# Kernel optimization log

Hardware: AMD Instinct MI355X
Metric: run time of the kernel (lower is better)

Reference implementation:

```python
import jax, jax.numpy as jnp
import numpy as np

B, M, E, IN, Q, OUT, H = 256, 2048, 128, 512, 512, 512, 64

def _lin(x, w, b):
    return x @ w.T + b

def setup_inputs() -> dict:
    key = jax.random.key(0)
    ks = jax.random.split(key, 20)
    d = {
        'read_weights': jax.random.uniform(ks[0], (B, M)),
        'write_weights': jax.random.uniform(ks[1], (B, M)),
        'usage': jax.random.uniform(ks[2], (B, M)),
        'free_gates': jax.random.uniform(ks[3], (B, M)),
        'x': jax.random.normal(ks[4], (B, 1, IN)),
        'query': jax.random.normal(ks[5], (B, 1, Q)),
        'memory': jax.random.normal(ks[6], (B, M, E)),
        'I_w': jax.random.normal(ks[7], (E, IN)) * 0.02, 'I_b': jnp.zeros((E,)),
        'W1_w': jax.random.normal(ks[8], (H, E)) * 0.02, 'W1_b': jnp.zeros((H,)),
        'W2_w': jax.random.normal(ks[9], (H, E)) * 0.02, 'W2_b': jnp.zeros((H,)),
        'R1_w': jax.random.normal(ks[10], (H, Q)) * 0.02, 'R1_b': jnp.zeros((H,)),
        'R2_w': jax.random.normal(ks[11], (H, E)) * 0.02, 'R2_b': jnp.zeros((H,)),
        'O_w': jax.random.normal(ks[12], (OUT, E)) * 0.02, 'O_b': jnp.zeros((OUT,)),
    }
    return d

def _allocation(read_weights, write_weights, usage, free_gates):
    u = 1e-5 + (1.0 - 1e-5) * usage
    psi = 1.0 - free_gates * read_weights
    u = u + write_weights - u * write_weights
    u = u * psi                                   # new usage [B, M]
    phi = jnp.argsort(u, axis=1)                  # ascending order indices
    sorted_u = jnp.take_along_axis(u, phi, axis=1)
    # NOTE: original uses inclusive cumprod (matches torch code exactly)
    sorted_alloc = (1.0 - sorted_u) * jnp.cumprod(sorted_u, axis=1)
    phi_rev = jnp.argsort(phi, axis=1)            # inverse permutation
    alloc = jnp.take_along_axis(sorted_alloc, phi_rev, axis=1)
    return u, alloc

def reference(read_weights, write_weights, usage, free_gates, x, query, memory,
              I_w, I_b, W1_w, W1_b, W2_w, W2_b, R1_w, R1_b, R2_w, R2_b, O_w, O_b):
    # ---- write ----
    emb = _lin(x, I_w, I_b)                       # [B,1,E]
    Wi = _lin(emb, W1_w, W1_b)                    # [B,1,H]
    Wm = _lin(memory, W2_w, W2_b)                 # [B,M,H]
    scores = jnp.einsum('bqh,bmh->bqm', Wi, Wm)   # [B,1,M]
    w_content = jax.nn.softmax(scores, axis=2)
    new_usage, alloc = _allocation(read_weights, write_weights, usage, free_gates)
    w = (w_content + alloc[:, None, :]) * 0.5     # [B,1,M]
    new_memory = memory + w.transpose(0, 2, 1) * emb  # [B,M,1]*[B,1,E]
    new_write_weights = w[:, 0, :]
    # ---- read ----
    Rq = _lin(query, R1_w, R1_b)                  # [B,1,H]
    Rm = _lin(new_memory, R2_w, R2_b)             # [B,M,H]
    rscores = jnp.einsum('bqh,bmh->bqm', Rq, Rm)
    wr = jax.nn.softmax(rscores, axis=2)          # [B,1,M]
    pooled = jnp.einsum('bm,bme->be', wr[:, 0, :], new_memory)
    output = _lin(pooled, O_w, O_b)               # [B,OUT]
    return ((wr[:, 0, :], new_write_weights, new_usage), output, new_memory)
```

## Files before the change

### kernel.cpp

```cpp
#include <hip/hip_runtime.h>
#include <hip/hip_bf16.h>

constexpr int B   = 256;
constexpr int M   = 2048;
constexpr int E   = 128;
constexpr int IN  = 512;
constexpr int Qd  = 512;
constexpr int OUTd= 512;
constexpr int H   = 64;

constexpr size_t OFF_WR = 0;
constexpr size_t OFF_W  = (size_t)B*M;
constexpr size_t OFF_U  = (size_t)2*B*M;
constexpr size_t OFF_Y  = (size_t)3*B*M;
constexpr size_t OFF_NM = OFF_Y + (size_t)B*OUTd;

__device__ __forceinline__ float bf2f(unsigned short u) {
    union { unsigned int i; float f; } v; v.i = ((unsigned int)u) << 16; return v.f;
}
__device__ __forceinline__ unsigned short f2bf(float f) {
    unsigned int x = __float_as_uint(f);
    unsigned int r = (x + 0x7fffu + ((x >> 16) & 1u)) >> 16;
    return (unsigned short)r;
}
__device__ __forceinline__ void unpack8(uint4 d, float* o) {
    o[0]=bf2f(d.x & 0xffff); o[1]=bf2f(d.x >> 16);
    o[2]=bf2f(d.y & 0xffff); o[3]=bf2f(d.y >> 16);
    o[4]=bf2f(d.z & 0xffff); o[5]=bf2f(d.z >> 16);
    o[6]=bf2f(d.w & 0xffff); o[7]=bf2f(d.w >> 16);
}
__device__ __forceinline__ uint4 pack8(const float* f) {
    uint4 d;
    d.x = (unsigned)f2bf(f[0]) | ((unsigned)f2bf(f[1]) << 16);
    d.y = (unsigned)f2bf(f[2]) | ((unsigned)f2bf(f[3]) << 16);
    d.z = (unsigned)f2bf(f[4]) | ((unsigned)f2bf(f[5]) << 16);
    d.w = (unsigned)f2bf(f[6]) | ((unsigned)f2bf(f[7]) << 16);
    return d;
}

__device__ __forceinline__ float ldf(const void* p, size_t i, int bf) {
    return bf ? bf2f(((const unsigned short*)p)[i]) : ((const float*)p)[i];
}
__device__ __forceinline__ void ld8(const void* p, size_t i, int bf, float* o) {
    if (bf) {
        uint4 d = *(const uint4*)((const unsigned short*)p + i);
        unpack8(d, o);
    } else {
        const float4* q = (const float4*)((const float*)p + i);
        float4 a = q[0], c = q[1];
        o[0]=a.x; o[1]=a.y; o[2]=a.z; o[3]=a.w;
        o[4]=c.x; o[5]=c.y; o[6]=c.z; o[7]=c.w;
    }
}
__device__ __forceinline__ void st1(void* p, size_t i, int bf, float v) {
    if (bf) ((unsigned short*)p)[i] = f2bf(v);
    else    ((float*)p)[i] = v;
}
__device__ __forceinline__ void st8(void* p, size_t i, int bf, const float* v) {
    if (bf) {
        *(uint4*)((unsigned short*)p + i) = pack8(v);
    } else {
        float4 a, c;
        a.x=v[0]; a.y=v[1]; a.z=v[2]; a.w=v[3];
        c.x=v[4]; c.y=v[5]; c.z=v[6]; c.w=v[7];
        float4* q = (float4*)((float*)p + i);
        q[0]=a; q[1]=c;
    }
}

__device__ __forceinline__ int detect_bf(const void* usage) {
    const int lane = threadIdx.x & 63;
    uint4 d = ((const uint4*)usage)[lane];
    float o[8]; unpack8(d, o);
    bool ok = true;
    #pragma unroll
    for (int j = 0; j < 8; ++j) ok = ok && (o[j] >= 0.0f && o[j] <= 1.0f);
    unsigned long long m = __ballot(ok);
    return (__popcll(m) >= 32) ? 1 : 0;
}

__device__ __forceinline__ float bmax4(float v, float* r4, int t) {
    #pragma unroll
    for (int m = 1; m < 64; m <<= 1) v = fmaxf(v, __shfl_xor(v, m, 64));
    __syncthreads();
    if ((t & 63) == 0) r4[t >> 6] = v;
    __syncthreads();
    return fmaxf(fmaxf(r4[0], r4[1]), fmaxf(r4[2], r4[3]));
}
__device__ __forceinline__ float bsum4(float v, float* r4, int t) {
    #pragma unroll
    for (int m = 1; m < 64; m <<= 1) v += __shfl_xor(v, m, 64);
    __syncthreads();
    if ((t & 63) == 0) r4[t >> 6] = v;
    __syncthreads();
    return (r4[0] + r4[1]) + (r4[2] + r4[3]);
}

__global__ __launch_bounds__(256) void kA_pre_alloc(
    const void* __restrict__ x,   const void* __restrict__ qy,
    const void* __restrict__ I_w, const void* __restrict__ I_b,
    const void* __restrict__ W1w, const void* __restrict__ W1b,
    const void* __restrict__ W2w, const void* __restrict__ W2b,
    const void* __restrict__ R1w, const void* __restrict__ R1b,
    const void* __restrict__ R2w, const void* __restrict__ R2b,
    const void* __restrict__ rw,  const void* __restrict__ ww,
    const void* __restrict__ us,  const void* __restrict__ fg,
    float* __restrict__ emb_ws, float* __restrict__ v_ws, float* __restrict__ u2_ws,
    float* __restrict__ c1_ws,  float* __restrict__ c2_ws, float* __restrict__ d2_ws,
    float* __restrict__ alloc_ws, void* __restrict__ dout)
{
    __shared__ unsigned long long sh64[M];
    __shared__ float scan[256];
    const int bf = detect_bf(us);
    const int t = threadIdx.x;

    if (blockIdx.x < B) {
        const int b = blockIdx.x;
        float* fsm  = (float*)sh64;
        float* xs   = fsm;
        float* qs   = fsm + 512;
        float* embs = fsm + 1024;
        float* wis  = fsm + 1152;
        float* rqs  = fsm + 1216;
        float* red  = scan;
        float uu = 0.f;

        for (int i = t; i < IN; i += 256) xs[i] = ldf(x,  (size_t)b*IN + i, bf);
        for (int i = t; i < Qd; i += 256) qs[i] = ldf(qy, (size_t)b*Qd + i, bf);
        __syncthreads();

        if (t < 128) {
            float acc = 0.f;
            for (int c = 0; c < IN/8; ++c) {
                float m8[8]; ld8(I_w, (size_t)t*IN + c*8, bf, m8);
                #pragma unroll
                for (int j = 0; j < 8; ++j) acc += m8[j] * xs[c*8 + j];
            }
            acc += ldf(I_b, t, bf);
            embs[t] = acc;
            emb_ws[(size_t)b*E + t] = acc;
        } else {
            int t2 = t - 128;
            if (t2 < H) {
                float rv = 0.f;
                for (int c = 0; c < Qd/8; ++c) {
                    float m8[8]; ld8(R1w, (size_t)t2*Qd + c*8, bf, m8);
                    #pragma unroll
                    for (int j = 0; j < 8; ++j) rv += m8[j] * qs[c*8 + j];
                }
                rv += ldf(R1b, t2, bf);
                rqs[t2] = rv;
            }
        }
        __syncthreads();

        if (t < H) {
            float wv = 0.f;
            for (int c = 0; c < E/8; ++c) {
                float m8[8]; ld8(W1w, (size_t)t*E + c*8, bf, m8);
                #pragma unroll
                for (int j = 0; j < 8; ++j) wv += m8[j] * embs[c*8 + j];
            }
            wv += ldf(W1b, t, bf);
            wis[t] = wv;
        } else if (t >= 128) {
            int t2 = t - 128;
            for (int h = 0; h < H; ++h) uu += ldf(R2w, (size_t)h*E + t2, bf) * rqs[h];
            u2_ws[(size_t)b*E + t2] = uu;
            red[t] = (t2 < H) ? rqs[t2] * ldf(R2b, t2, bf) : 0.f;
        }
        __syncthreads();

        if (t < 128) {
            float vv = 0.f;
            for (int h = 0; h < H; ++h) vv += ldf(W2w, (size_t)h*E + t, bf) * wis[h];
            v_ws[(size_t)b*E + t] = vv;
            red[t] = (t < H) ? wis[t] * ldf(W2b, t, bf) : 0.f;
        }
        __syncthreads();

        for (int off = 64; off > 0; off >>= 1) {
            if (t < off) red[t] += red[t + off];
            if (t >= 128 && t < 128 + off) red[t] += red[t + off];
            __syncthreads();
        }
        if (t == 0)   c1_ws[b] = red[0];
        if (t == 128) c2_ws[b] = red[128];
        __syncthreads();

        red[t] = (t >= 128) ? uu * embs[t - 128] : 0.f;
        __syncthreads();
        for (int off = 64; off > 0; off >>= 1) {
            if (t >= 128 && t < 128 + off) red[t] += red[t + off];
            __syncthreads();
        }
        if (t == 128) d2_ws[b] = red[128];

    } else {
        const int b = blockIdx.x - B;
        const size_t base = (size_t)b*M + (size_t)t*8;
        float r8[8], w8[8], u8[8], f8[8], nu[8];
        ld8(rw, base, bf, r8); ld8(ww, base, bf, w8);
        ld8(us, base, bf, u8); ld8(fg, base, bf, f8);

        unsigned long long key[8];
        #pragma unroll
        for (int q = 0; q < 8; ++q) {
            float u = 1e-5f + (1.0f - 1e-5f) * u8[q];
            float psi = 1.0f - f8[q] * r8[q];
            u = u + w8[q] - u * w8[q];
            u = u * psi;
            nu[q] = u;
            unsigned fb = __float_as_uint(u);
            fb = (fb & 0x80000000u) ? ~fb : (fb | 0x80000000u);
            key[q] = ((unsigned long long)fb << 32) | (unsigned)(t*8 + q);
        }
        st8(dout, OFF_U + base, bf, nu);

        for (int k = 2; k <= M; k <<= 1) {
            for (int j = k >> 1; j > 0; j >>= 1) {
                if (j >= 512) {
                    __syncthreads();
                    #pragma unroll
                    for (int q = 0; q < 8; ++q) sh64[t*8 + q] = key[q];
                    __syncthreads();
                    const bool up      = (((t << 3) & k) == 0);
                    const bool lower   = (((t << 3) & j) == 0);
                    const bool keepmin = (lower == up);
                    #pragma unroll
                    for (int q = 0; q < 8; ++q) {
                        unsigned long long o = sh64[(t*8 + q) ^ j];
                        bool take = keepmin ? (o < key[q]) : (o > key[q]);
                        if (take) key[q] = o;
                    }
                } else if (j >= 8) {
                    const int d = j >> 3;
                    const bool up      = (((t << 3) & k) == 0);
                    const bool keepmin = (((t & d) == 0) == up);
                    #pragma unroll
                    for (int q = 0; q < 8; ++q) {
                        unsigned long long o = __shfl_xor(key[q], d, 64);
                        bool take = keepmin ? (o < key[q]) : (o > key[q]);
                        if (take) key[q] = o;
                    }
                } else {
                    #pragma unroll
                    for (int q = 0; q < 8; ++q) {
                        if (!(q & j)) {
                            int p = q | j;
                            bool up = ((((t << 3) + q) & k) == 0);
                            unsigned long long a = key[q], c = key[p];
                            bool sw = up ? (a > c) : (a < c);
                            if (sw) { key[q] = c; key[p] = a; }
                        }
                    }
                }
            }
        }

        float su[8], lp[8]; int sidx[8];
        #pragma unroll
        for (int q = 0; q < 8; ++q) {
            unsigned fb = (unsigned)(key[q] >> 32);
            fb = (fb & 0x80000000u) ? (fb ^ 0x80000000u) : ~fb;
            su[q]   = __uint_as_float(fb);
            sidx[q] = (int)(key[q] & 0xffffffffu);
        }
        float run = 1.f;
        #pragma unroll
        for (int q = 0; q < 8; ++q) { run *= su[q]; lp[q] = run; }
        scan[t] = run;
        __syncthreads();
        for (int off = 1; off < 256; off <<= 1) {
            float val = scan[t];
            float oth = (t >= off) ? scan[t - off] : 1.0f;
            __syncthreads();
            scan[t] = val * oth;
            __syncthreads();
        }
        float pref = (t > 0) ? scan[t - 1] : 1.0f;
        #pragma unroll
        for (int q = 0; q < 8; ++q)
            alloc_ws[(size_t)b*M + sidx[q]] = (1.0f - su[q]) * (pref * lp[q]);
    }
}

__global__ __launch_bounds__(256) void kS_scores(
    const void* __restrict__ mem, const void* __restrict__ us,
    const float* __restrict__ v_ws, const float* __restrict__ u2_ws,
    const float* __restrict__ c1_ws,
    float* __restrict__ s1, float* __restrict__ s2)
{
    const int bf = detect_bf(us);
    const int blk = blockIdx.x;
    const int b = blk >> 4, chunk = blk & 15;
    const int t = threadIdx.x, l = t & 15, g = t >> 4;
    float v8[8], u8[8];
    {
        const float* vb = v_ws  + (size_t)b*E + l*8;
        const float* ub = u2_ws + (size_t)b*E + l*8;
        #pragma unroll
        for (int j = 0; j < 8; ++j) { v8[j] = vb[j]; u8[j] = ub[j]; }
    }
    const float cc1 = c1_ws[b];
    const size_t mbase = (size_t)b*M*E;
    const int row0 = chunk*128 + g;
    for (int it = 0; it < 8; ++it) {
        int row = row0 + it*16;
        float m8[8]; ld8(mem, mbase + (size_t)row*E + l*8, bf, m8);
        float p1 = 0.f, p2 = 0.f;
        #pragma unroll
        for (int j = 0; j < 8; ++j) { p1 += m8[j]*v8[j]; p2 += m8[j]*u8[j]; }
        #pragma unroll
        for (int mask = 8; mask > 0; mask >>= 1) {
            p1 += __shfl_xor(p1, mask, 16);
            p2 += __shfl_xor(p2, mask, 16);
        }
        if (l == 0) {
            s1[(size_t)b*M + row] = p1 + cc1;
            s2[(size_t)b*M + row] = p2;
        }
    }
}

__global__ __launch_bounds__(256) void kU_update(
    const void* __restrict__ mem, const void* __restrict__ us,
    const float* __restrict__ emb_ws, const float* __restrict__ alloc_ws,
    const float* __restrict__ s1, const float* __restrict__ s2,
    const float* __restrict__ c2_ws, const float* __restrict__ d2_ws,
    float* __restrict__ pooled_p, void* __restrict__ dout)
{
    __shared__ float wsh[M];
    __shared__ float wrsh[M];
    __shared__ float pw[4][E];
    __shared__ float r4[4];
    const int bf = detect_bf(us);
    const int rblk = (B*16 - 1) - (int)blockIdx.x;
    const int b = rblk >> 4, chunk = rblk & 15;
    const int t = threadIdx.x, l = t & 15, g = t >> 4;

    const float* s1b = s1 + (size_t)b*M;
    const float* s2b = s2 + (size_t)b*M;
    float sv[8];
    float lmax = -3.4e38f;
    #pragma unroll
    for (int s = 0; s < 8; ++s) { sv[s] = s1b[s*256 + t]; lmax = fmaxf(lmax, sv[s]); }
    float gmax = bmax4(lmax, r4, t);
    float lsum = 0.f;
    #pragma unroll
    for (int s = 0; s < 8; ++s) { float e = expf(sv[s] - gmax); sv[s] = e; lsum += e; }
    float inv = 1.0f / bsum4(lsum, r4, t);

    const float dd = d2_ws[b], cc = c2_ws[b];
    float rs[8];
    #pragma unroll
    for (int s = 0; s < 8; ++s) {
        int m = s*256 + t;
        float wv = 0.5f * (sv[s] * inv + alloc_ws[(size_t)b*M + m]);
        wsh[m] = wv;
        rs[s] = s2b[m] + wv * dd + cc;
        if (chunk == 0) st1(dout, OFF_W + (size_t)b*M + m, bf, wv);
    }

    lmax = -3.4e38f;
    #pragma unroll
    for (int s = 0; s < 8; ++s) lmax = fmaxf(lmax, rs[s]);
    gmax = bmax4(lmax, r4, t);
    lsum = 0.f;
    #pragma unroll
    for (int s = 0; s < 8; ++s) { float e = expf(rs[s] - gmax); rs[s] = e; lsum += e; }
    float inv2 = 1.0f / bsum4(lsum, r4, t);
    #pragma unroll
    for (int s = 0; s < 8; ++s) {
        int m = s*256 + t;
        float wrv = rs[s] * inv2;
        wrsh[m] = wrv;
        if (chunk == 0) st1(dout, OFF_WR + (size_t)b*M + m, bf, wrv);
    }
    __syncthreads();

    float e8[8];
    {
        const float* eb = emb_ws + (size_t)b*E + l*8;
        #pragma unroll
        for (int j = 0; j < 8; ++j) e8[j] = eb[j];
    }
    float acc[8] = {0,0,0,0,0,0,0,0};
    const size_t mbase = (size_t)b*M*E;
    const int row0 = chunk*128 + g;
    for (int it = 0; it < 8; ++it) {
        int row = row0 + it*16;
        size_t off = mbase + (size_t)row*E + l*8;
        float m8[8]; ld8(mem, off, bf, m8);
        const float wv  = wsh[row];
        const float wrv = wrsh[row];
        float n8[8];
        #pragma unroll
        for (int j = 0; j < 8; ++j) {
            n8[j] = m8[j] + wv * e8[j];
            acc[j] += wrv * n8[j];
        }
        st8(dout, OFF_NM + off, bf, n8);
    }
    #pragma unroll
    for (int j = 0; j < 8; ++j) {
        acc[j] += __shfl_xor(acc[j], 16, 64);
        acc[j] += __shfl_xor(acc[j], 32, 64);
    }
    const int wid = t >> 6;
    if ((t & 63) < 16) {
        const int l0 = t & 15;
        #pragma unroll
        for (int j = 0; j < 8; ++j) pw[wid][l0*8 + j] = acc[j];
    }
    __syncthreads();
    if (t < E)
        pooled_p[((size_t)b*16 + chunk)*E + t] = pw[0][t] + pw[1][t] + pw[2][t] + pw[3][t];
}

__global__ __launch_bounds__(512) void kO_out(
    const float* __restrict__ pooled_p,
    const void* __restrict__ O_w, const void* __restrict__ O_b,
    const void* __restrict__ us, void* __restrict__ dout)
{
    __shared__ float ps[E];
    const int bf = detect_bf(us);
    const int b = blockIdx.x, t = threadIdx.x;
    if (t < E) {
        float s = 0.f;
        #pragma unroll
        for (int c = 0; c < 16; ++c) s += pooled_p[((size_t)b*16 + c)*E + t];
        ps[t] = s;
    }
    __syncthreads();
    float a = 0.f;
    for (int c = 0; c < E/8; ++c) {
        float m8[8]; ld8(O_w, (size_t)t*E + c*8, bf, m8);
        #pragma unroll
        for (int j = 0; j < 8; ++j) a += m8[j] * ps[c*8 + j];
    }
    a += ldf(O_b, t, bf);
    st1(dout, OFF_Y + (size_t)b*OUTd + t, bf, a);
}

extern "C" void kernel_launch(void* const* d_in, const int* in_sizes, int n_in,
                              void* d_out, int out_size, void* d_ws, size_t ws_size,
                              hipStream_t stream)
{
    const void* rw  = d_in[0];
    const void* ww  = d_in[1];
    const void* us  = d_in[2];
    const void* fg  = d_in[3];
    const void* x   = d_in[4];
    const void* qy  = d_in[5];
    const void* mem = d_in[6];
    const void* I_w = d_in[7];
    const void* I_b = d_in[8];
    const void* W1w = d_in[9];
    const void* W1b = d_in[10];
    const void* W2w = d_in[11];
    const void* W2b = d_in[12];
    const void* R1w = d_in[13];
    const void* R1b = d_in[14];
    const void* R2w = d_in[15];
    const void* R2b = d_in[16];
    const void* O_w = d_in[17];
    const void* O_b = d_in[18];

    float* fbase    = (float*)d_ws;
    float* emb_ws   = fbase;
    float* v_ws     = emb_ws + (size_t)B*E;
    float* u2_ws    = v_ws   + (size_t)B*E;
    float* c1_ws    = u2_ws  + (size_t)B*E;
    float* c2_ws    = c1_ws  + B;
    float* d2_ws    = c2_ws  + B;
    float* alloc_ws = d2_ws  + B;
    float* s1_ws    = alloc_ws + (size_t)B*M;
    float* s2_ws    = s1_ws    + (size_t)B*M;
    float* pooled_p = s2_ws    + (size_t)B*M;

    kA_pre_alloc<<<2*B, 256, 0, stream>>>(x, qy, I_w, I_b, W1w, W1b, W2w, W2b,
                                          R1w, R1b, R2w, R2b, rw, ww, us, fg,
                                          emb_ws, v_ws, u2_ws, c1_ws, c2_ws, d2_ws,
                                          alloc_ws, d_out);
    kS_scores<<<B*16, 256, 0, stream>>>(mem, us, v_ws, u2_ws, c1_ws, s1_ws, s2_ws);
    kU_update<<<B*16, 256, 0, stream>>>(mem, us, emb_ws, alloc_ws, s1_ws, s2_ws,
                                        c2_ws, d2_ws, pooled_p, d_out);
    kO_out   <<<B,    512, 0, stream>>>(pooled_p, O_w, O_b, us, d_out);
}
```

Before: 670.9 us.

## Restructure pipeline: overlap allocation sort with score pass, precompute softmax stats

Splits the projection prologue into its own kernel and merges the per-batch allocation sort with the memory score pass in one launch, so sorting blocks run alongside streaming blocks. Softmax max and normalizer for both the write and read weights are computed once per batch in a new small stats kernel. The update kernel then no longer re-reduces all 2048 scores in each of its 16 chunk blocks; each block only evaluates its own 128 rows. This adds one extra launch and a small read of the score arrays in exchange for removing redundant per-chunk reductions and large shared-memory buffers.

```diff
diff --git a/kernel.cpp b/kernel.cpp
--- a/kernel.cpp
+++ b/kernel.cpp
@@ -96,18 +96,102 @@
     return (r4[0] + r4[1]) + (r4[2] + r4[3]);
 }
 
-__global__ __launch_bounds__(256) void kA_pre_alloc(
+__global__ __launch_bounds__(256) void k1_pre(
     const void* __restrict__ x,   const void* __restrict__ qy,
     const void* __restrict__ I_w, const void* __restrict__ I_b,
     const void* __restrict__ W1w, const void* __restrict__ W1b,
     const void* __restrict__ W2w, const void* __restrict__ W2b,
     const void* __restrict__ R1w, const void* __restrict__ R1b,
     const void* __restrict__ R2w, const void* __restrict__ R2b,
-    const void* __restrict__ rw,  const void* __restrict__ ww,
-    const void* __restrict__ us,  const void* __restrict__ fg,
+    const void* __restrict__ us,
     float* __restrict__ emb_ws, float* __restrict__ v_ws, float* __restrict__ u2_ws,
-    float* __restrict__ c1_ws,  float* __restrict__ c2_ws, float* __restrict__ d2_ws,
-    float* __restrict__ alloc_ws, void* __restrict__ dout)
+    float* __restrict__ c1_ws,  float* __restrict__ c2_ws, float* __restrict__ d2_ws)
+{
+    const int bf = detect_bf(us);
+    __shared__ float xs[IN], qs[Qd], embs[E], wis[H], rqs[H], red[256];
+    const int b = blockIdx.x, t = threadIdx.x;
+    float uu = 0.f;
+
+    for (int i = t; i < IN; i += 256) xs[i] = ldf(x,  (size_t)b*IN + i, bf);
+    for (int i = t; i < Qd; i += 256) qs[i] = ldf(qy, (size_t)b*Qd + i, bf);
+    __syncthreads();
+
+    if (t < 128) {
+        float acc = 0.f;
+        for (int c = 0; c < IN/8; ++c) {
+            float m8[8]; ld8(I_w, (size_t)t*IN + c*8, bf, m8);
+            #pragma unroll
+            for (int j = 0; j < 8; ++j) acc += m8[j] * xs[c*8 + j];
+        }
+        acc += ldf(I_b, t, bf);
+        embs[t] = acc;
+        emb_ws[(size_t)b*E + t] = acc;
+    } else {
+        int t2 = t - 128;
+        if (t2 < H) {
+            float rv = 0.f;
+            for (int c = 0; c < Qd/8; ++c) {
+                float m8[8]; ld8(R1w, (size_t)t2*Qd + c*8, bf, m8);
+                #pragma unroll
+                for (int j = 0; j < 8; ++j) rv += m8[j] * qs[c*8 + j];
+            }
+            rv += ldf(R1b, t2, bf);
+            rqs[t2] = rv;
+        }
+    }
+    __syncthreads();
+
+    if (t < H) {
+        float wv = 0.f;
+        for (int c = 0; c < E/8; ++c) {
+            float m8[8]; ld8(W1w, (size_t)t*E + c*8, bf, m8);
+            #pragma unroll
+            for (int j = 0; j < 8; ++j) wv += m8[j] * embs[c*8 + j];
+        }
+        wv += ldf(W1b, t, bf);
+        wis[t] = wv;
+    } else if (t >= 128) {
+        int t2 = t - 128;
+        for (int h = 0; h < H; ++h) uu += ldf(R2w, (size_t)h*E + t2, bf) * rqs[h];
+        u2_ws[(size_t)b*E + t2] = uu;
+        red[t] = (t2 < H) ? rqs[t2] * ldf(R2b, t2, bf) : 0.f;
+    }
+    __syncthreads();
+
+    if (t < 128) {
+        float vv = 0.f;
+        for (int h = 0; h < H; ++h) vv += ldf(W2w, (size_t)h*E + t, bf) * wis[h];
+        v_ws[(size_t)b*E + t] = vv;
+        red[t] = (t < H) ? wis[t] * ldf(W2b, t, bf) : 0.f;
+    }
+    __syncthreads();
+
+    for (int off = 64; off > 0; off >>= 1) {
+        if (t < off) red[t] += red[t + off];
+        if (t >= 128 && t < 128 + off) red[t] += red[t + off];
+        __syncthreads();
+    }
+    if (t == 0)   c1_ws[b] = red[0];
+    if (t == 128) c2_ws[b] = red[128];
+    __syncthreads();
+
+    red[t] = (t >= 128) ? uu * embs[t - 128] : 0.f;
+    __syncthreads();
+    for (int off = 64; off > 0; off >>= 1) {
+        if (t >= 128 && t < 128 + off) red[t] += red[t + off];
+        __syncthreads();
+    }
+    if (t == 128) d2_ws[b] = red[128];
+}
+
+__global__ __launch_bounds__(256) void kB_alloc_scores(
+    const void* __restrict__ rw, const void* __restrict__ ww,
+    const void* __restrict__ us, const void* __restrict__ fg,
+    const void* __restrict__ mem,
+    const float* __restrict__ v_ws, const float* __restrict__ u2_ws,
+    const float* __restrict__ c1_ws,
+    float* __restrict__ alloc_ws, float* __restrict__ s1, float* __restrict__ s2,
+    void* __restrict__ dout)
 {
     __shared__ unsigned long long sh64[M];
     __shared__ float scan[256];
@@ -116,88 +200,6 @@
 
     if (blockIdx.x < B) {
         const int b = blockIdx.x;
-        float* fsm  = (float*)sh64;
-        float* xs   = fsm;
-        float* qs   = fsm + 512;
-        float* embs = fsm + 1024;
-        float* wis  = fsm + 1152;
-        float* rqs  = fsm + 1216;
-        float* red  = scan;
-        float uu = 0.f;
-
-        for (int i = t; i < IN; i += 256) xs[i] = ldf(x,  (size_t)b*IN + i, bf);
-        for (int i = t; i < Qd; i += 256) qs[i] = ldf(qy, (size_t)b*Qd + i, bf);
-        __syncthreads();
-
-        if (t < 128) {
-            float acc = 0.f;
-            for (int c = 0; c < IN/8; ++c) {
-                float m8[8]; ld8(I_w, (size_t)t*IN + c*8, bf, m8);
-                #pragma unroll
-                for (int j = 0; j < 8; ++j) acc += m8[j] * xs[c*8 + j];
-            }
-            acc += ldf(I_b, t, bf);
-            embs[t] = acc;
-            emb_ws[(size_t)b*E + t] = acc;
-        } else {
-            int t2 = t - 128;
-            if (t2 < H) {
-                float rv = 0.f;
-                for (int c = 0; c < Qd/8; ++c) {
-                    float m8[8]; ld8(R1w, (size_t)t2*Qd + c*8, bf, m8);
-                    #pragma unroll
-                    for (int j = 0; j < 8; ++j) rv += m8[j] * qs[c*8 + j];
-                }
-                rv += ldf(R1b, t2, bf);
-                rqs[t2] = rv;
-            }
-        }
-        __syncthreads();
-
-        if (t < H) {
-            float wv = 0.f;
-            for (int c = 0; c < E/8; ++c) {
-                float m8[8]; ld8(W1w, (size_t)t*E + c*8, bf, m8);
-                #pragma unroll
-                for (int j = 0; j < 8; ++j) wv += m8[j] * embs[c*8 + j];
-            }
-            wv += ldf(W1b, t, bf);
-            wis[t] = wv;
-        } else if (t >= 128) {
-            int t2 = t - 128;
-            for (int h = 0; h < H; ++h) uu += ldf(R2w, (size_t)h*E + t2, bf) * rqs[h];
-            u2_ws[(size_t)b*E + t2] = uu;
-            red[t] = (t2 < H) ? rqs[t2] * ldf(R2b, t2, bf) : 0.f;
-        }
-        __syncthreads();
-
-        if (t < 128) {
-            float vv = 0.f;
-            for (int h = 0; h < H; ++h) vv += ldf(W2w, (size_t)h*E + t, bf) * wis[h];
-            v_ws[(size_t)b*E + t] = vv;
-            red[t] = (t < H) ? wis[t] * ldf(W2b, t, bf) : 0.f;
-        }
-        __syncthreads();
-
-        for (int off = 64; off > 0; off >>= 1) {
-            if (t < off) red[t] += red[t + off];
-            if (t >= 128 && t < 128 + off) red[t] += red[t + off];
-            __syncthreads();
-        }
-        if (t == 0)   c1_ws[b] = red[0];
-        if (t == 128) c2_ws[b] = red[128];
-        __syncthreads();
-
-        red[t] = (t >= 128) ? uu * embs[t - 128] : 0.f;
-        __syncthreads();
-        for (int off = 64; off > 0; off >>= 1) {
-            if (t >= 128 && t < 128 + off) red[t] += red[t + off];
-            __syncthreads();
-        }
-        if (t == 128) d2_ws[b] = red[128];
-
-    } else {
-        const int b = blockIdx.x - B;
         const size_t base = (size_t)b*M + (size_t)t*8;
         float r8[8], w8[8], u8[8], f8[8], nu[8];
         ld8(rw, base, bf, r8); ld8(ww, base, bf, w8);
@@ -282,100 +284,115 @@
         #pragma unroll
         for (int q = 0; q < 8; ++q)
             alloc_ws[(size_t)b*M + sidx[q]] = (1.0f - su[q]) * (pref * lp[q]);
-    }
-}
-
-__global__ __launch_bounds__(256) void kS_scores(
-    const void* __restrict__ mem, const void* __restrict__ us,
-    const float* __restrict__ v_ws, const float* __restrict__ u2_ws,
-    const float* __restrict__ c1_ws,
-    float* __restrict__ s1, float* __restrict__ s2)
+
+    } else {
+        const int blk = blockIdx.x - B;
+        const int b = blk >> 4, chunk = blk & 15;
+        const int l = t & 15, g = t >> 4;
+        float v8[8], u8[8];
+        {
+            const float* vb = v_ws  + (size_t)b*E + l*8;
+            const float* ub = u2_ws + (size_t)b*E + l*8;
+            #pragma unroll
+            for (int j = 0; j < 8; ++j) { v8[j] = vb[j]; u8[j] = ub[j]; }
+        }
+        const float cc1 = c1_ws[b];
+        const size_t mbase = (size_t)b*M*E;
+        const int row0 = chunk*128 + g;
+        for (int it = 0; it < 8; ++it) {
+            int row = row0 + it*16;
+            float m8[8]; ld8(mem, mbase + (size_t)row*E + l*8, bf, m8);
+            float p1 = 0.f, p2 = 0.f;
+            #pragma unroll
+            for (int j = 0; j < 8; ++j) { p1 += m8[j]*v8[j]; p2 += m8[j]*u8[j]; }
+            #pragma unroll
+            for (int mask = 8; mask > 0; mask >>= 1) {
+                p1 += __shfl_xor(p1, mask, 16);
+                p2 += __shfl_xor(p2, mask, 16);
+            }
+            if (l == 0) {
+                s1[(size_t)b*M + row] = p1 + cc1;
+                s2[(size_t)b*M + row] = p2;
+            }
+        }
+    }
+}
+
+__global__ __launch_bounds__(256) void k4_stats(
+    const float* __restrict__ s1, const float* __restrict__ s2,
+    const float* __restrict__ alloc_ws,
+    const float* __restrict__ c2_ws, const float* __restrict__ d2_ws,
+    float* __restrict__ stats_ws)
 {
-    const int bf = detect_bf(us);
-    const int blk = blockIdx.x;
-    const int b = blk >> 4, chunk = blk & 15;
-    const int t = threadIdx.x, l = t & 15, g = t >> 4;
-    float v8[8], u8[8];
-    {
-        const float* vb = v_ws  + (size_t)b*E + l*8;
-        const float* ub = u2_ws + (size_t)b*E + l*8;
-        #pragma unroll
-        for (int j = 0; j < 8; ++j) { v8[j] = vb[j]; u8[j] = ub[j]; }
-    }
-    const float cc1 = c1_ws[b];
-    const size_t mbase = (size_t)b*M*E;
-    const int row0 = chunk*128 + g;
-    for (int it = 0; it < 8; ++it) {
-        int row = row0 + it*16;
-        float m8[8]; ld8(mem, mbase + (size_t)row*E + l*8, bf, m8);
-        float p1 = 0.f, p2 = 0.f;
-        #pragma unroll
-        for (int j = 0; j < 8; ++j) { p1 += m8[j]*v8[j]; p2 += m8[j]*u8[j]; }
-        #pragma unroll
-        for (int mask = 8; mask > 0; mask >>= 1) {
-            p1 += __shfl_xor(p1, mask, 16);
-            p2 += __shfl_xor(p2, mask, 16);
-        }
-        if (l == 0) {
-            s1[(size_t)b*M + row] = p1 + cc1;
-            s2[(size_t)b*M + row] = p2;
-        }
-    }
-}
-
-__global__ __launch_bounds__(256) void kU_update(
+    __shared__ float r4[4];
+    const int b = blockIdx.x, t = threadIdx.x;
+    const float* s1b = s1 + (size_t)b*M;
+    const float* s2b = s2 + (size_t)b*M;
+
+    float sv[8];
+    float lmax = -3.4e38f;
+    #pragma unroll
+    for (int s = 0; s < 8; ++s) { sv[s] = s1b[s*256 + t]; lmax = fmaxf(lmax, sv[s]); }
+    const float gmax1 = bmax4(lmax, r4, t);
+    float lsum = 0.f;
+    #pragma unroll
+    for (int s = 0; s < 8; ++s) { float e = expf(sv[s] - gmax1); sv[s] = e; lsum += e; }
+    const float inv1 = 1.0f / bsum4(lsum, r4, t);
+
+    const float dd = d2_ws[b], cc = c2_ws[b];
+    float rs[8];
+    lmax = -3.4e38f;
+    #pragma unroll
+    for (int s = 0; s < 8; ++s) {
+        int m = s*256 + t;
+        float wv = 0.5f * (sv[s] * inv1 + alloc_ws[(size_t)b*M + m]);
+        rs[s] = s2b[m] + wv * dd + cc;
+        lmax = fmaxf(lmax, rs[s]);
+    }
+    const float gmax2 = bmax4(lmax, r4, t);
+    lsum = 0.f;
+    #pragma unroll
+    for (int s = 0; s < 8; ++s) lsum += expf(rs[s] - gmax2);
+    const float inv2 = 1.0f / bsum4(lsum, r4, t);
+
+    if (t == 0) {
+        stats_ws[b*4 + 0] = gmax1;
+        stats_ws[b*4 + 1] = inv1;
+        stats_ws[b*4 + 2] = gmax2;
+        stats_ws[b*4 + 3] = inv2;
+    }
+}
+
+__global__ __launch_bounds__(256) void k5_update(
     const void* __restrict__ mem, const void* __restrict__ us,
     const float* __restrict__ emb_ws, const float* __restrict__ alloc_ws,
     const float* __restrict__ s1, const float* __restrict__ s2,
     const float* __restrict__ c2_ws, const float* __restrict__ d2_ws,
+    const float* __restrict__ stats_ws,
     float* __restrict__ pooled_p, void* __restrict__ dout)
 {
-    __shared__ float wsh[M];
-    __shared__ float wrsh[M];
+    __shared__ float wsh[128];
+    __shared__ float wrsh[128];
     __shared__ float pw[4][E];
-    __shared__ float r4[4];
     const int bf = detect_bf(us);
     const int rblk = (B*16 - 1) - (int)blockIdx.x;
     const int b = rblk >> 4, chunk = rblk & 15;
     const int t = threadIdx.x, l = t & 15, g = t >> 4;
 
-    const float* s1b = s1 + (size_t)b*M;
-    const float* s2b = s2 + (size_t)b*M;
-    float sv[8];
-    float lmax = -3.4e38f;
-    #pragma unroll
-    for (int s = 0; s < 8; ++s) { sv[s] = s1b[s*256 + t]; lmax = fmaxf(lmax, sv[s]); }
-    float gmax = bmax4(lmax, r4, t);
-    float lsum = 0.f;
-    #pragma unroll
-    for (int s = 0; s < 8; ++s) { float e = expf(sv[s] - gmax); sv[s] = e; lsum += e; }
-    float inv = 1.0f / bsum4(lsum, r4, t);
-
+    const float gmax1 = stats_ws[b*4 + 0], inv1 = stats_ws[b*4 + 1];
+    const float gmax2 = stats_ws[b*4 + 2], inv2 = stats_ws[b*4 + 3];
     const float dd = d2_ws[b], cc = c2_ws[b];
-    float rs[8];
-    #pragma unroll
-    for (int s = 0; s < 8; ++s) {
-        int m = s*256 + t;
-        float wv = 0.5f * (sv[s] * inv + alloc_ws[(size_t)b*M + m]);
-        wsh[m] = wv;
-        rs[s] = s2b[m] + wv * dd + cc;
-        if (chunk == 0) st1(dout, OFF_W + (size_t)b*M + m, bf, wv);
-    }
-
-    lmax = -3.4e38f;
-    #pragma unroll
-    for (int s = 0; s < 8; ++s) lmax = fmaxf(lmax, rs[s]);
-    gmax = bmax4(lmax, r4, t);
-    lsum = 0.f;
-    #pragma unroll
-    for (int s = 0; s < 8; ++s) { float e = expf(rs[s] - gmax); rs[s] = e; lsum += e; }
-    float inv2 = 1.0f / bsum4(lsum, r4, t);
-    #pragma unroll
-    for (int s = 0; s < 8; ++s) {
-        int m = s*256 + t;
-        float wrv = rs[s] * inv2;
-        wrsh[m] = wrv;
-        if (chunk == 0) st1(dout, OFF_WR + (size_t)b*M + m, bf, wrv);
+
+    if (t < 128) {
+        const size_t m = (size_t)b*M + chunk*128 + t;
+        float e1  = expf(s1[m] - gmax1);
+        float wv  = 0.5f * (e1 * inv1 + alloc_ws[m]);
+        float rsv = s2[m] + wv * dd + cc;
+        float wrv = expf(rsv - gmax2) * inv2;
+        wsh[t]  = wv;
+        wrsh[t] = wrv;
+        st1(dout, OFF_W  + m, bf, wv);
+        st1(dout, OFF_WR + m, bf, wrv);
     }
     __syncthreads();
 
@@ -387,13 +404,13 @@
     }
     float acc[8] = {0,0,0,0,0,0,0,0};
     const size_t mbase = (size_t)b*M*E;
-    const int row0 = chunk*128 + g;
     for (int it = 0; it < 8; ++it) {
-        int row = row0 + it*16;
+        int lr = g + it*16;
+        int row = chunk*128 + lr;
         size_t off = mbase + (size_t)row*E + l*8;
         float m8[8]; ld8(mem, off, bf, m8);
-        const float wv  = wsh[row];
-        const float wrv = wrsh[row];
+        const float wv  = wsh[lr];
+        const float wrv = wrsh[lr];
         float n8[8];
         #pragma unroll
         for (int j = 0; j < 8; ++j) {
@@ -474,17 +491,21 @@
     float* c1_ws    = u2_ws  + (size_t)B*E;
     float* c2_ws    = c1_ws  + B;
     float* d2_ws    = c2_ws  + B;
-    float* alloc_ws = d2_ws  + B;
+    float* stats_ws = d2_ws  + B;
+    float* alloc_ws = stats_ws + (size_t)4*B;
     float* s1_ws    = alloc_ws + (size_t)B*M;
     float* s2_ws    = s1_ws    + (size_t)B*M;
     float* pooled_p = s2_ws    + (size_t)B*M;
 
-    kA_pre_alloc<<<2*B, 256, 0, stream>>>(x, qy, I_w, I_b, W1w, W1b, W2w, W2b,
-                                          R1w, R1b, R2w, R2b, rw, ww, us, fg,
-                                          emb_ws, v_ws, u2_ws, c1_ws, c2_ws, d2_ws,
-                                          alloc_ws, d_out);
-    kS_scores<<<B*16, 256, 0, stream>>>(mem, us, v_ws, u2_ws, c1_ws, s1_ws, s2_ws);
-    kU_update<<<B*16, 256, 0, stream>>>(mem, us, emb_ws, alloc_ws, s1_ws, s2_ws,
-                                        c2_ws, d2_ws, pooled_p, d_out);
-    kO_out   <<<B,    512, 0, stream>>>(pooled_p, O_w, O_b, us, d_out);
-}
+    k1_pre  <<<B,        256, 0, stream>>>(x, qy, I_w, I_b, W1w, W1b, W2w, W2b,
+                                           R1w, R1b, R2w, R2b, us,
+                                           emb_ws, v_ws, u2_ws, c1_ws, c2_ws, d2_ws);
+    kB_alloc_scores<<<B + B*16, 256, 0, stream>>>(rw, ww, us, fg, mem,
+                                           v_ws, u2_ws, c1_ws,
+                                           alloc_ws, s1_ws, s2_ws, d_out);
+    k4_stats<<<B,        256, 0, stream>>>(s1_ws, s2_ws, alloc_ws, c2_ws, d2_ws,
+                                           stats_ws);
+    k5_update<<<B*16,    256, 0, stream>>>(mem, us, emb_ws, alloc_ws, s1_ws, s2_ws,
+                                           c2_ws, d2_ws, stats_ws, pooled_p, d_out);
+    kO_out  <<<B,        512, 0, stream>>>(pooled_p, O_w, O_b, us, d_out);
+}
```

Result: faster. 625.1 us (-6.8%).
